# Kernel optimization log

Hardware: AMD Instinct MI355X
Metric: run time of the kernel (lower is better)

## Reference

```python
import jax, jax.numpy as jnp
import numpy as np


def setup_inputs() -> dict:
    key = jax.random.key(0)
    k0, k1 = jax.random.split(key)
    b, n, m, e = 8, 2048, 2048, 1024
    mat_0 = jax.random.normal(k0, (b, n, e), dtype=jnp.float32)
    mat_1 = jax.random.normal(k1, (b, m, e), dtype=jnp.float32)
    return {"mat_0": mat_0, "mat_1": mat_1}


def reference(mat_0, mat_1):
    # Original tiles to [b,n,m,e], multiplies, and sums over e.
    # Mathematically identical to a batched QK^T matmul: [b,n,m].
    return jnp.einsum('bne,bme->bnm', mat_0, mat_1)
```

## Files before the change

### kernel.cpp

```cpp
#include <hip/hip_runtime.h>

typedef __attribute__((ext_vector_type(8))) short short8;
typedef __attribute__((ext_vector_type(4))) float f32x4;
typedef __attribute__((ext_vector_type(2))) unsigned int u32x2;
typedef unsigned short u16;

static constexpr int BATCH = 8;
static constexpr int NDIM  = 2048;
static constexpr int MDIM  = 2048;
static constexpr int EDIM  = 1024;
static constexpr int BM    = 128;
static constexpr int BN    = 128;
static constexpr int BK    = 64;

#define BAR() do { asm volatile("" ::: "memory"); \
                   __builtin_amdgcn_s_barrier(); \
                   asm volatile("" ::: "memory"); } while (0)
#define WFENCE() asm volatile("s_waitcnt lgkmcnt(0)" ::: "memory")

__global__ __launch_bounds__(256, 2)
void bmm_fused_kernel(const float* __restrict__ A, const float* __restrict__ B,
                      float* __restrict__ C) {
  __shared__ u16 sh[2][2][BM * BK];

  const int tid  = threadIdx.x;
  const int lane = tid & 63;
  const int wave = tid >> 6;
  const int quad = lane >> 4;
  const int ml   = lane & 15;
  const int wrow = (wave >> 1) * 64;
  const int wcol = (wave & 1) * 64;

  const int flat  = (int)blockIdx.x + 16 * (int)blockIdx.y + 256 * (int)blockIdx.z;
  const int nf    = (flat & 7) * 256 + (flat >> 3);
  const int batch = nf >> 8;
  const int trow  = (nf >> 4) & 15;
  const int tcol  = nf & 15;

  const float* Ab = A + (size_t)batch * NDIM * EDIM + (size_t)trow * BM * EDIM;
  const float* Bb = B + (size_t)batch * MDIM * EDIM + (size_t)tcol * BN * EDIM;

  const int rowb = tid >> 4;
  const int ci   = tid & 15;
  const int colf = ci * 4;
  const int swzoff = (((ci >> 1) ^ (rowb & 7)) << 3) | ((ci & 1) << 2);
  const float* pA = Ab + (size_t)rowb * EDIM + colf;
  const float* pB = Bb + (size_t)rowb * EDIM + colf;

  const int aOff = (wrow + ml) * 64;
  const int bOff = (wcol + ml) * 64;
  const int kc0 = ((quad    ) ^ (ml & 7)) * 8;
  const int kc1 = ((quad + 4) ^ (ml & 7)) * 8;

  short8 ar[2][2], br[2][2];
  f32x4 acc[4][4] = {};
  f32x4 X[4];

#define ISS(P, u, t) do {                                                      \
    const float* _p = (P) + (size_t)((u) * 64) * EDIM + (size_t)(t) * BK;      \
    X[0] = *(const f32x4*)(_p);                                                \
    X[1] = *(const f32x4*)(_p + (size_t)16 * EDIM);                            \
    X[2] = *(const f32x4*)(_p + (size_t)32 * EDIM);                            \
    X[3] = *(const f32x4*)(_p + (size_t)48 * EDIM);                            \
  } while (0)

#define WRT(buf, ab, u) do {                                                   \
    _Pragma("unroll")                                                          \
    for (int _j = 0; _j < 4; ++_j) {                                           \
      unsigned _lo, _hi;                                                       \
      asm("v_cvt_pk_bf16_f32 %0, %1, %2"                                       \
          : "=v"(_lo) : "v"(X[_j][0]), "v"(X[_j][1]));                         \
      asm("v_cvt_pk_bf16_f32 %0, %1, %2"                                       \
          : "=v"(_hi) : "v"(X[_j][2]), "v"(X[_j][3]));                         \
      u32x2 _u; _u[0] = _lo; _u[1] = _hi;                                      \
      *(u32x2*)&sh[buf][ab][((u) * 64 + rowb + _j * 16) * 64 + swzoff] = _u;   \
    } } while (0)

#define LDA(buf, mh) do {                                                      \
    _Pragma("unroll")                                                          \
    for (int _s = 0; _s < 2; ++_s) {                                           \
      ar[_s][0] = *(const short8*)&sh[buf][0][aOff + ((mh)*32 + _s*16)*64 + kc0];\
      ar[_s][1] = *(const short8*)&sh[buf][0][aOff + ((mh)*32 + _s*16)*64 + kc1];\
    } } while (0)

#define LDB(buf, nh) do {                                                      \
    _Pragma("unroll")                                                          \
    for (int _s = 0; _s < 2; ++_s) {                                           \
      br[_s][0] = *(const short8*)&sh[buf][1][bOff + ((nh)*32 + _s*16)*64 + kc0];\
      br[_s][1] = *(const short8*)&sh[buf][1][bOff + ((nh)*32 + _s*16)*64 + kc1];\
    } } while (0)

#define MM(mh, nh) do {                                                        \
    __builtin_amdgcn_s_setprio(1);                                             \
    _Pragma("unroll")                                                          \
    for (int _sa = 0; _sa < 2; ++_sa)                                          \
      _Pragma("unroll")                                                        \
      for (int _sb = 0; _sb < 2; ++_sb)                                        \
        _Pragma("unroll")                                                      \
        for (int _ks = 0; _ks < 2; ++_ks)                                      \
          acc[(mh)*2 + _sa][(nh)*2 + _sb] = __builtin_amdgcn_mfma_f32_16x16x32_bf16(\
              ar[_sa][_ks], br[_sb][_ks], acc[(mh)*2 + _sa][(nh)*2 + _sb], 0, 0, 0);\
    __builtin_amdgcn_s_setprio(0);                                             \
  } while (0)

  ISS(pA, 0, 0); WRT(0, 0, 0);
  ISS(pA, 1, 0); WRT(0, 0, 1);
  ISS(pB, 0, 0); WRT(0, 1, 0);
  ISS(pB, 1, 0); WRT(0, 1, 1);
  ISS(pA, 0, 1);
  WFENCE();
  BAR();

#pragma unroll 1
  for (int i = 0; i < 8; ++i) {
    const int t1  = 2 * i + 1;
    const int tp0 = (2 * i + 2 < 15) ? 2 * i + 2 : 15;
    const int tp1 = (2 * i + 3 < 15) ? 2 * i + 3 : 15;
    LDA(0, 0); LDB(0, 0);
    WRT(1, 0, 0); ISS(pA, 1, t1);
    BAR(); MM(0, 0); WFENCE(); BAR();
    LDB(0, 1);
    WRT(1, 0, 1); ISS(pB, 0, t1);
    BAR(); MM(0, 1); WFENCE(); BAR();
    LDA(0, 1);
    WRT(1, 1, 0); ISS(pB, 1, t1);
    BAR(); MM(1, 1); WFENCE(); BAR();
    LDB(0, 0);
    WRT(1, 1, 1); ISS(pA, 0, tp0);
    BAR(); MM(1, 0); WFENCE(); BAR();
    LDA(1, 0); LDB(1, 0);
    WRT(0, 0, 0); ISS(pA, 1, tp0);
    BAR(); MM(0, 0); WFENCE(); BAR();
    LDB(1, 1);
    WRT(0, 0, 1); ISS(pB, 0, tp0);
    BAR(); MM(0, 1); WFENCE(); BAR();
    LDA(1, 1);
    WRT(0, 1, 0); ISS(pB, 1, tp0);
    BAR(); MM(1, 1); WFENCE(); BAR();
    LDB(1, 0);
    WRT(0, 1, 1); ISS(pA, 0, tp1);
    BAR(); MM(1, 0); WFENCE(); BAR();
  }

  float* Cb = C + (size_t)batch * NDIM * MDIM
                + (size_t)(trow * BM + wrow + quad * 4) * MDIM
                + (tcol * BN + wcol + ml);
#pragma unroll
  for (int mi = 0; mi < 4; ++mi) {
#pragma unroll
    for (int ni = 0; ni < 4; ++ni) {
      float* cp = Cb + (size_t)(mi * 16) * MDIM + ni * 16;
#pragma unroll
      for (int r = 0; r < 4; ++r)
        cp[(size_t)r * MDIM] = acc[mi][ni][r];
    }
  }
#undef ISS
#undef WRT
#undef LDA
#undef LDB
#undef MM
}

extern "C" void kernel_launch(void* const* d_in, const int* in_sizes, int n_in,
                              void* d_out, int out_size, void* d_ws, size_t ws_size,
                              hipStream_t stream) {
  const float* A = (const float*)d_in[0];
  const float* B = (const float*)d_in[1];
  float*       C = (float*)d_out;
  (void)d_ws; (void)ws_size;

  dim3 grid(MDIM / BN, NDIM / BM, BATCH);
  bmm_fused_kernel<<<grid, dim3(256), 0, stream>>>(A, B, C);
}
```

Baseline: 334.1 us.

## Restructure GEMM main loop with four staging register sets and fewer barriers

Replaces the single f32 staging register set with four (A and B halves), so each half-tile is loaded from global memory a full k-step ahead of its conversion and LDS write. The main loop now runs once per k-tile in two phases instead of eight sub-phases per two tiles. All B fragments for a k-tile are loaded from LDS once, and each MFMA block covers a full row stripe, which cuts barriers and redundant LDS reads. The cost is more VGPR pressure from the extra staging and fragment registers, and less interleaving of MFMA with memory traffic inside each phase.

```diff
diff --git a/kernel.cpp b/kernel.cpp
--- a/kernel.cpp
+++ b/kernel.cpp
@@ -52,26 +52,26 @@
   const int kc0 = ((quad    ) ^ (ml & 7)) * 8;
   const int kc1 = ((quad + 4) ^ (ml & 7)) * 8;
 
-  short8 ar[2][2], br[2][2];
+  short8 ar[2][2], br[4][2];
   f32x4 acc[4][4] = {};
-  f32x4 X[4];
+  f32x4 SA0[4], SA1[4], SB0[4], SB1[4];
 
-#define ISS(P, u, t) do {                                                      \
+#define ISS(Sp, P, u, t) do {                                                  \
     const float* _p = (P) + (size_t)((u) * 64) * EDIM + (size_t)(t) * BK;      \
-    X[0] = *(const f32x4*)(_p);                                                \
-    X[1] = *(const f32x4*)(_p + (size_t)16 * EDIM);                            \
-    X[2] = *(const f32x4*)(_p + (size_t)32 * EDIM);                            \
-    X[3] = *(const f32x4*)(_p + (size_t)48 * EDIM);                            \
+    Sp[0] = *(const f32x4*)(_p);                                               \
+    Sp[1] = *(const f32x4*)(_p + (size_t)16 * EDIM);                           \
+    Sp[2] = *(const f32x4*)(_p + (size_t)32 * EDIM);                           \
+    Sp[3] = *(const f32x4*)(_p + (size_t)48 * EDIM);                           \
   } while (0)
 
-#define WRT(buf, ab, u) do {                                                   \
+#define WRT(Sp, buf, ab, u) do {                                               \
     _Pragma("unroll")                                                          \
     for (int _j = 0; _j < 4; ++_j) {                                           \
       unsigned _lo, _hi;                                                       \
       asm("v_cvt_pk_bf16_f32 %0, %1, %2"                                       \
-          : "=v"(_lo) : "v"(X[_j][0]), "v"(X[_j][1]));                         \
+          : "=v"(_lo) : "v"(Sp[_j][0]), "v"(Sp[_j][1]));                       \
       asm("v_cvt_pk_bf16_f32 %0, %1, %2"                                       \
-          : "=v"(_hi) : "v"(X[_j][2]), "v"(X[_j][3]));                         \
+          : "=v"(_hi) : "v"(Sp[_j][2]), "v"(Sp[_j][3]));                       \
       u32x2 _u; _u[0] = _lo; _u[1] = _hi;                                      \
       *(u32x2*)&sh[buf][ab][((u) * 64 + rowb + _j * 16) * 64 + swzoff] = _u;   \
     } } while (0)
@@ -83,63 +83,49 @@
       ar[_s][1] = *(const short8*)&sh[buf][0][aOff + ((mh)*32 + _s*16)*64 + kc1];\
     } } while (0)
 
-#define LDB(buf, nh) do {                                                      \
+#define LDBALL(buf) do {                                                       \
     _Pragma("unroll")                                                          \
-    for (int _s = 0; _s < 2; ++_s) {                                           \
-      br[_s][0] = *(const short8*)&sh[buf][1][bOff + ((nh)*32 + _s*16)*64 + kc0];\
-      br[_s][1] = *(const short8*)&sh[buf][1][bOff + ((nh)*32 + _s*16)*64 + kc1];\
+    for (int _n = 0; _n < 4; ++_n) {                                           \
+      br[_n][0] = *(const short8*)&sh[buf][1][bOff + _n*1024 + kc0];           \
+      br[_n][1] = *(const short8*)&sh[buf][1][bOff + _n*1024 + kc1];           \
     } } while (0)
 
-#define MM(mh, nh) do {                                                        \
+#define MM2(mh) do {                                                           \
     __builtin_amdgcn_s_setprio(1);                                             \
     _Pragma("unroll")                                                          \
     for (int _sa = 0; _sa < 2; ++_sa)                                          \
       _Pragma("unroll")                                                        \
-      for (int _sb = 0; _sb < 2; ++_sb)                                        \
+      for (int _n = 0; _n < 4; ++_n)                                           \
         _Pragma("unroll")                                                      \
         for (int _ks = 0; _ks < 2; ++_ks)                                      \
-          acc[(mh)*2 + _sa][(nh)*2 + _sb] = __builtin_amdgcn_mfma_f32_16x16x32_bf16(\
-              ar[_sa][_ks], br[_sb][_ks], acc[(mh)*2 + _sa][(nh)*2 + _sb], 0, 0, 0);\
+          acc[(mh)*2 + _sa][_n] = __builtin_amdgcn_mfma_f32_16x16x32_bf16(     \
+              ar[_sa][_ks], br[_n][_ks], acc[(mh)*2 + _sa][_n], 0, 0, 0);      \
     __builtin_amdgcn_s_setprio(0);                                             \
   } while (0)
 
-  ISS(pA, 0, 0); WRT(0, 0, 0);
-  ISS(pA, 1, 0); WRT(0, 0, 1);
-  ISS(pB, 0, 0); WRT(0, 1, 0);
-  ISS(pB, 1, 0); WRT(0, 1, 1);
-  ISS(pA, 0, 1);
+  ISS(SA0, pA, 0, 0); ISS(SA1, pA, 1, 0); ISS(SB0, pB, 0, 0); ISS(SB1, pB, 1, 0);
+  WRT(SA0, 0, 0, 0);  WRT(SA1, 0, 0, 1);  WRT(SB0, 0, 1, 0);  WRT(SB1, 0, 1, 1);
+  ISS(SA0, pA, 0, 1); ISS(SA1, pA, 1, 1); ISS(SB0, pB, 0, 1); ISS(SB1, pB, 1, 1);
   WFENCE();
   BAR();
 
 #pragma unroll 1
-  for (int i = 0; i < 8; ++i) {
-    const int t1  = 2 * i + 1;
-    const int tp0 = (2 * i + 2 < 15) ? 2 * i + 2 : 15;
-    const int tp1 = (2 * i + 3 < 15) ? 2 * i + 3 : 15;
-    LDA(0, 0); LDB(0, 0);
-    WRT(1, 0, 0); ISS(pA, 1, t1);
-    BAR(); MM(0, 0); WFENCE(); BAR();
-    LDB(0, 1);
-    WRT(1, 0, 1); ISS(pB, 0, t1);
-    BAR(); MM(0, 1); WFENCE(); BAR();
-    LDA(0, 1);
-    WRT(1, 1, 0); ISS(pB, 1, t1);
-    BAR(); MM(1, 1); WFENCE(); BAR();
-    LDB(0, 0);
-    WRT(1, 1, 1); ISS(pA, 0, tp0);
-    BAR(); MM(1, 0); WFENCE(); BAR();
-    LDA(1, 0); LDB(1, 0);
-    WRT(0, 0, 0); ISS(pA, 1, tp0);
-    BAR(); MM(0, 0); WFENCE(); BAR();
-    LDB(1, 1);
-    WRT(0, 0, 1); ISS(pB, 0, tp0);
-    BAR(); MM(0, 1); WFENCE(); BAR();
-    LDA(1, 1);
-    WRT(0, 1, 0); ISS(pB, 1, tp0);
-    BAR(); MM(1, 1); WFENCE(); BAR();
-    LDB(1, 0);
-    WRT(0, 1, 1); ISS(pA, 0, tp1);
-    BAR(); MM(1, 0); WFENCE(); BAR();
+  for (int u = 0; u < 16; ++u) {
+    const int b  = u & 1;
+    const int w  = b ^ 1;
+    const int tp = (u < 14) ? u + 2 : 15;
+    LDA(b, 0); LDBALL(b);
+    MM2(0);
+    __builtin_amdgcn_sched_barrier(0);
+    WRT(SA0, w, 0, 0); WRT(SA1, w, 0, 1);
+    ISS(SA0, pA, 0, tp); ISS(SA1, pA, 1, tp);
+    WFENCE(); BAR();
+    LDA(b, 1);
+    MM2(1);
+    __builtin_amdgcn_sched_barrier(0);
+    WRT(SB0, w, 1, 0); WRT(SB1, w, 1, 1);
+    ISS(SB0, pB, 0, tp); ISS(SB1, pB, 1, tp);
+    WFENCE(); BAR();
   }
 
   float* Cb = C + (size_t)batch * NDIM * MDIM
@@ -158,8 +144,8 @@
 #undef ISS
 #undef WRT
 #undef LDA
-#undef LDB
-#undef MM
+#undef LDBALL
+#undef MM2
 }
 
 extern "C" void kernel_launch(void* const* d_in, const int* in_sizes, int n_in,
```

Result: faster. 317.8 us (-4.9%).
